# Kernel tuning notes

Measured on AMD Instinct MI355X. Metric: run time of the kernel, lower is better.

The kernel has to match this reference:

```python
import jax, jax.numpy as jnp
import numpy as np

N = 50000          # nodes
E = 800000         # edges (avg degree 16)
DIN, DH, DOUT = 128, 256, 40


def setup_inputs() -> dict:
    key = jax.random.key(0)
    ks = jax.random.split(key, 6)
    x = jax.random.normal(ks[0], (N, DIN), dtype=jnp.float32)
    edge_index = jax.random.randint(ks[1], (2, E), 0, N, dtype=jnp.int32)
    W1 = jax.random.normal(ks[2], (DIN, DH), dtype=jnp.float32) * (1.0 / np.sqrt(DIN))
    b1 = jnp.zeros((DH,), dtype=jnp.float32)
    W2 = jax.random.normal(ks[3], (DH, DOUT), dtype=jnp.float32) * (1.0 / np.sqrt(DH))
    b2 = jnp.zeros((DOUT,), dtype=jnp.float32)
    return {"x": x, "edge_index": edge_index, "W1": W1, "b1": b1, "W2": W2, "b2": b2}


def gcn_conv(x, src, dst, W, b, n):
    # PyG GCNConv: add self-loops, symmetric normalization D^-1/2 A D^-1/2,
    # dense projection, scatter-sum aggregation, then bias.
    deg = jax.ops.segment_sum(jnp.ones_like(dst, dtype=x.dtype), dst, num_segments=n)
    dinv = jnp.where(deg > 0, jax.lax.rsqrt(deg), 0.0)
    norm = dinv[src] * dinv[dst]          # [E+N]
    h = x @ W                              # [N, dout] dense GEMM
    msg = h[src] * norm[:, None]          # gather + scale, [E+N, dout]
    out = jax.ops.segment_sum(msg, dst, num_segments=n)  # scatter-add
    return out + b


def reference(x, edge_index, W1, b1, W2, b2):
    n = x.shape[0]
    loops = jnp.arange(n, dtype=edge_index.dtype)
    src = jnp.concatenate([edge_index[0], loops])
    dst = jnp.concatenate([edge_index[1], loops])
    h = jax.nn.relu(gcn_conv(x, src, dst, W1, b1, n))
    h = gcn_conv(h, src, dst, W2, b2, n)
    return jax.nn.log_softmax(h, axis=1)
```

## Files before the change

kernel.cpp:

```cpp
#include <hip/hip_runtime.h>
#include <math.h>

#define DIN 128
#define DH 256
#define DOUT 40
#define MLP_ROWS 64

#define BSH 7
#define BNODES 128
#define NBUK 391
#define CAP 4096
#define PART_T 512
#define PART_EPB 8
#define PART_CHUNK (PART_T * PART_EPB)

typedef short short8 __attribute__((ext_vector_type(8)));
typedef float f32x4 __attribute__((ext_vector_type(4)));

__device__ inline unsigned f2bf(float f) {
    unsigned u = __float_as_uint(f);
    return (u + 0x7fffu + ((u >> 16) & 1u)) >> 16;
}
__device__ inline float bflo(unsigned u) { return __uint_as_float(u << 16); }
__device__ inline float bfhi(unsigned u) { return __uint_as_float(u & 0xffff0000u); }


__global__ __launch_bounds__(PART_T) void k_partition(
    const int* __restrict__ src, const int* __restrict__ dst,
    int* __restrict__ gcur, unsigned* __restrict__ raw, int E) {
    __shared__ int hist[NBUK];
    __shared__ int lbase[NBUK];
    int tid = threadIdx.x;
    int base_e = blockIdx.x * PART_CHUNK;

    for (int i = tid; i < NBUK; i += PART_T) hist[i] = 0;
    __syncthreads();

    int s[PART_EPB], d[PART_EPB];
#pragma unroll
    for (int k = 0; k < PART_EPB; ++k) {
        int e = base_e + k * PART_T + tid;
        if (e < E) { s[k] = src[e]; d[k] = dst[e]; }
        else d[k] = -1;
    }
#pragma unroll
    for (int k = 0; k < PART_EPB; ++k)
        if (d[k] >= 0) atomicAdd(&hist[d[k] >> BSH], 1);
    __syncthreads();

    for (int b = tid; b < NBUK; b += PART_T) {
        int c = hist[b];
        lbase[b] = c ? atomicAdd(&gcur[b], c) : 0;
    }
    __syncthreads();
    for (int i = tid; i < NBUK; i += PART_T) hist[i] = 0;
    __syncthreads();

#pragma unroll
    for (int k = 0; k < PART_EPB; ++k) {
        if (d[k] >= 0) {
            int b = d[k] >> BSH;
            int pos = lbase[b] + atomicAdd(&hist[b], 1);
            if (pos < (b + 1) * CAP)
                raw[pos] = ((unsigned)(d[k] & (BNODES - 1)) << 16) | (unsigned)s[k];
        }
    }
}

__global__ __launch_bounds__(256) void k_bucket_csr(
    const unsigned* __restrict__ raw, const int* __restrict__ gcur,
    int* __restrict__ row_ptr, int* __restrict__ row_end,
    float* __restrict__ dinv, unsigned short* __restrict__ esrc, int n) {
    __shared__ int cnt[BNODES];
    __shared__ int scn[BNODES];
    __shared__ int lcur[BNODES];
    int b = blockIdx.x;
    int tid = threadIdx.x;
    int base = b * CAP;
    int size = gcur[b] - base;
    if (size > CAP) size = CAP;

    if (tid < BNODES) cnt[tid] = 0;
    __syncthreads();
    for (int i = tid; i < size; i += 256)
        atomicAdd(&cnt[raw[base + i] >> 16], 1);
    __syncthreads();

    if (tid < BNODES) scn[tid] = cnt[tid];
    __syncthreads();
    for (int off = 1; off < BNODES; off <<= 1) {
        int v = 0;
        if (tid < BNODES && tid >= off) v = scn[tid - off];
        __syncthreads();
        if (tid < BNODES) scn[tid] += v;
        __syncthreads();
    }
    if (tid < BNODES) {
        int excl = scn[tid] - cnt[tid];
        lcur[tid] = excl;
        int g = b * BNODES + tid;
        if (g < n) {
            row_ptr[g] = base + excl;
            row_end[g] = base + excl + cnt[tid];
            dinv[g]    = rsqrtf((float)cnt[tid] + 1.0f);
        }
    }
    __syncthreads();
    for (int i = tid; i < size; i += 256) {
        unsigned rec = raw[base + i];
        int pos = atomicAdd(&lcur[rec >> 16], 1);
        esrc[base + pos] = (unsigned short)(rec & 0xffffu);
    }
}

__global__ void k_prep(const float* __restrict__ x, const float* __restrict__ W1,
                       const float* __restrict__ W2, unsigned* __restrict__ xb,
                       unsigned* __restrict__ w1t, unsigned* __restrict__ w2t,
                       int* __restrict__ gcur, int n64) {
    int i = blockIdx.x * blockDim.x + threadIdx.x;
    if (i < n64) {
        float2 v = ((const float2*)x)[i];
        xb[i] = f2bf(v.x) | (f2bf(v.y) << 16);
        return;
    }
    i -= n64;
    if (i < 256 * 64) {
        int c = i >> 6;
        int kk = (i & 63) * 2;
        w1t[i] = f2bf(W1[kk * DH + c]) | (f2bf(W1[(kk + 1) * DH + c]) << 16);
        return;
    }
    i -= 256 * 64;
    if (i < 48 * 128) {
        int col = i >> 7;
        int kk = (i & 127) * 2;
        float a = (col < DOUT) ? W2[kk * DOUT + col] : 0.f;
        float bb = (col < DOUT) ? W2[(kk + 1) * DOUT + col] : 0.f;
        w2t[i] = f2bf(a) | (f2bf(bb) << 16);
        return;
    }
    i -= 48 * 128;
    if (i < NBUK) gcur[i] = i * CAP;
}

__global__ void k_gather_agg1(const uint2* __restrict__ xb2,
                              const unsigned short* __restrict__ esrc,
                              const int* __restrict__ row_ptr, const int* __restrict__ row_end,
                              const float* __restrict__ dinv, uint2* __restrict__ axb2, int n) {
    int wid = (blockIdx.x * blockDim.x + threadIdx.x) >> 6;
    int lane = threadIdx.x & 63;
    int node = wid * 2 + (lane >> 5);
    int hl = lane & 31;
    if (node >= n) return;
    int beg = row_ptr[node], end = row_end[node];
    float dn = dinv[node];
    uint2 sv = xb2[(size_t)node * 32 + hl];
    float ax = dn * bflo(sv.x), ay = dn * bfhi(sv.x);
    float az = dn * bflo(sv.y), aw = dn * bfhi(sv.y);
    int t = beg;
    for (; t + 8 <= end; t += 8) {
        int s0 = esrc[t],     s1 = esrc[t + 1], s2 = esrc[t + 2], s3 = esrc[t + 3];
        int s4 = esrc[t + 4], s5 = esrc[t + 5], s6 = esrc[t + 6], s7 = esrc[t + 7];
        float w0 = dinv[s0], w1 = dinv[s1], w2 = dinv[s2], w3 = dinv[s3];
        float w4 = dinv[s4], w5 = dinv[s5], w6 = dinv[s6], w7 = dinv[s7];
        uint2 v0 = xb2[(size_t)s0 * 32 + hl];
        uint2 v1 = xb2[(size_t)s1 * 32 + hl];
        uint2 v2 = xb2[(size_t)s2 * 32 + hl];
        uint2 v3 = xb2[(size_t)s3 * 32 + hl];
        uint2 v4 = xb2[(size_t)s4 * 32 + hl];
        uint2 v5 = xb2[(size_t)s5 * 32 + hl];
        uint2 v6 = xb2[(size_t)s6 * 32 + hl];
        uint2 v7 = xb2[(size_t)s7 * 32 + hl];
        ax += w0 * bflo(v0.x) + w1 * bflo(v1.x) + w2 * bflo(v2.x) + w3 * bflo(v3.x)
            + w4 * bflo(v4.x) + w5 * bflo(v5.x) + w6 * bflo(v6.x) + w7 * bflo(v7.x);
        ay += w0 * bfhi(v0.x) + w1 * bfhi(v1.x) + w2 * bfhi(v2.x) + w3 * bfhi(v3.x)
            + w4 * bfhi(v4.x) + w5 * bfhi(v5.x) + w6 * bfhi(v6.x) + w7 * bfhi(v7.x);
        az += w0 * bflo(v0.y) + w1 * bflo(v1.y) + w2 * bflo(v2.y) + w3 * bflo(v3.y)
            + w4 * bflo(v4.y) + w5 * bflo(v5.y) + w6 * bflo(v6.y) + w7 * bflo(v7.y);
        aw += w0 * bfhi(v0.y) + w1 * bfhi(v1.y) + w2 * bfhi(v2.y) + w3 * bfhi(v3.y)
            + w4 * bfhi(v4.y) + w5 * bfhi(v5.y) + w6 * bfhi(v6.y) + w7 * bfhi(v7.y);
    }
    for (; t + 4 <= end; t += 4) {
        int s0 = esrc[t], s1 = esrc[t + 1], s2 = esrc[t + 2], s3 = esrc[t + 3];
        float w0 = dinv[s0], w1 = dinv[s1], w2 = dinv[s2], w3 = dinv[s3];
        uint2 v0 = xb2[(size_t)s0 * 32 + hl];
        uint2 v1 = xb2[(size_t)s1 * 32 + hl];
        uint2 v2 = xb2[(size_t)s2 * 32 + hl];
        uint2 v3 = xb2[(size_t)s3 * 32 + hl];
        ax += w0 * bflo(v0.x) + w1 * bflo(v1.x) + w2 * bflo(v2.x) + w3 * bflo(v3.x);
        ay += w0 * bfhi(v0.x) + w1 * bfhi(v1.x) + w2 * bfhi(v2.x) + w3 * bfhi(v3.x);
        az += w0 * bflo(v0.y) + w1 * bflo(v1.y) + w2 * bflo(v2.y) + w3 * bflo(v3.y);
        aw += w0 * bfhi(v0.y) + w1 * bfhi(v1.y) + w2 * bfhi(v2.y) + w3 * bfhi(v3.y);
    }
    for (; t < end; ++t) {
        int s = esrc[t];
        float w = dinv[s];
        uint2 v = xb2[(size_t)s * 32 + hl];
        ax += w * bflo(v.x); ay += w * bfhi(v.x);
        az += w * bflo(v.y); aw += w * bfhi(v.y);
    }
    ax *= dn; ay *= dn; az *= dn; aw *= dn;
    axb2[(size_t)node * 32 + hl] =
        make_uint2(f2bf(ax) | (f2bf(ay) << 16), f2bf(az) | (f2bf(aw) << 16));
}

__global__ __launch_bounds__(256) void k_mlp_mfma(
    const unsigned short* __restrict__ axb, const unsigned short* __restrict__ w1t,
    const float* __restrict__ b1, const unsigned short* __restrict__ w2t,
    unsigned short* __restrict__ pb, int n) {
    __shared__ __align__(16) char smem[65536];
    const int tid = threadIdx.x;
    const int lane = tid & 63;
    const int wv = tid >> 6;
    const int l15 = lane & 15;
    const int lg = lane >> 4;
    const int blockRow = blockIdx.x * MLP_ROWS;

    for (int i = tid; i < 256 * 16; i += 256) {
        int j = i >> 4, seg = i & 15;
        short8 v = *(const short8*)(w1t + j * 128 + seg * 8);
        *(short8*)(smem + j * 256 + ((seg * 16) ^ ((j & 7) << 4))) = v;
    }

    int arow = blockRow + wv * 16 + l15;
    if (arow >= n) arow = n - 1;
    const unsigned short* axp = axb + (size_t)arow * DIN + lg * 8;
    short8 aF[4];
#pragma unroll
    for (int ks = 0; ks < 4; ++ks) aF[ks] = *(const short8*)(axp + ks * 32);

    __syncthreads();

    f32x4 acc[16];
#pragma unroll
    for (int nt = 0; nt < 16; ++nt) acc[nt] = (f32x4){0.f, 0.f, 0.f, 0.f};
#pragma unroll
    for (int ks = 0; ks < 4; ++ks) {
        int kb = (ks * 32 + lg * 8) * 2;
#pragma unroll
        for (int nt = 0; nt < 16; ++nt) {
            int j = nt * 16 + l15;
            short8 bF = *(const short8*)(smem + j * 256 + (kb ^ ((j & 7) << 4)));
            acc[nt] = __builtin_amdgcn_mfma_f32_16x16x32_bf16(aF[ks], bF, acc[nt], 0, 0, 0);
        }
    }
    __syncthreads();

    unsigned short* s_h = (unsigned short*)smem;
    unsigned short* s_w2 = (unsigned short*)(smem + 33792);

#pragma unroll
    for (int nt = 0; nt < 16; ++nt) {
        int col = nt * 16 + l15;
        float bias = b1[col];
#pragma unroll
        for (int r = 0; r < 4; ++r) {
            int row = wv * 16 + lg * 4 + r;
            float v = fmaxf(acc[nt][r] + bias, 0.f);
            s_h[row * 264 + col] = (unsigned short)f2bf(v);
        }
    }
    for (int i = tid; i < 48 * 32; i += 256) {
        int j = i >> 5, seg = i & 31;
        short8 v = *(const short8*)(w2t + j * 256 + seg * 8);
        *(short8*)(s_w2 + j * 264 + seg * 8) = v;
    }
    __syncthreads();

    f32x4 acc2[3];
#pragma unroll
    for (int t = 0; t < 3; ++t) acc2[t] = (f32x4){0.f, 0.f, 0.f, 0.f};
#pragma unroll
    for (int ks = 0; ks < 8; ++ks) {
        int k = ks * 32 + lg * 8;
        short8 aH = *(const short8*)(s_h + (wv * 16 + l15) * 264 + k);
#pragma unroll
        for (int t = 0; t < 3; ++t) {
            short8 bF = *(const short8*)(s_w2 + (t * 16 + l15) * 264 + k);
            acc2[t] = __builtin_amdgcn_mfma_f32_16x16x32_bf16(aH, bF, acc2[t], 0, 0, 0);
        }
    }
#pragma unroll
    for (int t = 0; t < 3; ++t) {
        int col = t * 16 + l15;
        if (col < DOUT) {
#pragma unroll
            for (int r = 0; r < 4; ++r) {
                int row = blockRow + wv * 16 + lg * 4 + r;
                if (row < n) pb[(size_t)row * DOUT + col] = (unsigned short)f2bf(acc2[t][r]);
            }
        }
    }
}

__global__ void k_gather2_lsm(const unsigned* __restrict__ pbu,
                              const unsigned short* __restrict__ esrc,
                              const int* __restrict__ row_ptr, const int* __restrict__ row_end,
                              const float* __restrict__ dinv, const float* __restrict__ b2,
                              float* __restrict__ out, int n) {
    int wid = (blockIdx.x * blockDim.x + threadIdx.x) >> 6;
    int lane = threadIdx.x & 63;
    int node = wid * 2 + (lane >> 5);
    int hl = lane & 31;
    if (node >= n) return;
    int beg = row_ptr[node], end = row_end[node];
    float dn = dinv[node];
    int cl = (hl < 20) ? hl : 0;
    unsigned pv = pbu[(size_t)node * 20 + cl];
    float accx = dn * bflo(pv);
    float accy = dn * bfhi(pv);
    int t = beg;
    for (; t + 8 <= end; t += 8) {
        int s0 = esrc[t],     s1 = esrc[t + 1], s2 = esrc[t + 2], s3 = esrc[t + 3];
        int s4 = esrc[t + 4], s5 = esrc[t + 5], s6 = esrc[t + 6], s7 = esrc[t + 7];
        float w0 = dinv[s0], w1 = dinv[s1], w2 = dinv[s2], w3 = dinv[s3];
        float w4 = dinv[s4], w5 = dinv[s5], w6 = dinv[s6], w7 = dinv[s7];
        unsigned p0 = pbu[(size_t)s0 * 20 + cl];
        unsigned p1 = pbu[(size_t)s1 * 20 + cl];
        unsigned p2 = pbu[(size_t)s2 * 20 + cl];
        unsigned p3 = pbu[(size_t)s3 * 20 + cl];
        unsigned p4 = pbu[(size_t)s4 * 20 + cl];
        unsigned p5 = pbu[(size_t)s5 * 20 + cl];
        unsigned p6 = pbu[(size_t)s6 * 20 + cl];
        unsigned p7 = pbu[(size_t)s7 * 20 + cl];
        accx += w0 * bflo(p0) + w1 * bflo(p1) + w2 * bflo(p2) + w3 * bflo(p3)
              + w4 * bflo(p4) + w5 * bflo(p5) + w6 * bflo(p6) + w7 * bflo(p7);
        accy += w0 * bfhi(p0) + w1 * bfhi(p1) + w2 * bfhi(p2) + w3 * bfhi(p3)
              + w4 * bfhi(p4) + w5 * bfhi(p5) + w6 * bfhi(p6) + w7 * bfhi(p7);
    }
    for (; t + 4 <= end; t += 4) {
        int s0 = esrc[t], s1 = esrc[t + 1], s2 = esrc[t + 2], s3 = esrc[t + 3];
        float w0 = dinv[s0], w1 = dinv[s1], w2 = dinv[s2], w3 = dinv[s3];
        unsigned p0 = pbu[(size_t)s0 * 20 + cl];
        unsigned p1 = pbu[(size_t)s1 * 20 + cl];
        unsigned p2 = pbu[(size_t)s2 * 20 + cl];
        unsigned p3 = pbu[(size_t)s3 * 20 + cl];
        accx += w0 * bflo(p0) + w1 * bflo(p1) + w2 * bflo(p2) + w3 * bflo(p3);
        accy += w0 * bfhi(p0) + w1 * bfhi(p1) + w2 * bfhi(p2) + w3 * bfhi(p3);
    }
    for (; t < end; ++t) {
        int s = esrc[t];
        float w = dinv[s];
        unsigned p = pbu[(size_t)s * 20 + cl];
        accx += w * bflo(p);
        accy += w * bfhi(p);
    }
    float vx = -INFINITY, vy = -INFINITY;
    if (hl < 20) {
        float2 bv = ((const float2*)b2)[hl];
        vx = dn * accx + bv.x;
        vy = dn * accy + bv.y;
    }
    float m = fmaxf(vx, vy);
#pragma unroll
    for (int off = 16; off; off >>= 1) m = fmaxf(m, __shfl_xor(m, off, 32));
    float ex = (hl < 20) ? (expf(vx - m) + expf(vy - m)) : 0.f;
    float ssum = ex;
#pragma unroll
    for (int off = 16; off; off >>= 1) ssum += __shfl_xor(ssum, off, 32);
    float ls = logf(ssum);
    if (hl < 20)
        ((float2*)(out + (size_t)node * DOUT))[hl] = make_float2(vx - m - ls, vy - m - ls);
}

extern "C" void kernel_launch(void* const* d_in, const int* in_sizes, int n_in,
                              void* d_out, int out_size, void* d_ws, size_t ws_size,
                              hipStream_t stream) {
    const float* x  = (const float*)d_in[0];
    const int*   ei = (const int*)d_in[1];
    const float* W1 = (const float*)d_in[2];
    const float* b1 = (const float*)d_in[3];
    const float* W2 = (const float*)d_in[4];
    const float* b2 = (const float*)d_in[5];
    float* out = (float*)d_out;

    int n = in_sizes[0] / DIN;
    int E = in_sizes[1] / 2;
    const int* src = ei;
    const int* dst = ei + E;

    int*            gcur    = (int*)d_ws;
    int*            row_ptr = gcur + 512;
    int*            row_end = row_ptr + n;
    float*          dinv    = (float*)(row_end + n);
    unsigned*       w1t     = (unsigned*)(dinv + n);
    unsigned*       w2t     = w1t + 16384;
    unsigned*       raw     = w2t + 6144;
    unsigned short* esrc    = (unsigned short*)(raw + (size_t)NBUK * CAP);
    unsigned*       xb      = (unsigned*)(esrc + (size_t)NBUK * CAP);
    unsigned*       axb     = xb + (size_t)n * 64;
    unsigned short* pb      = (unsigned short*)xb;

    const int B = 256;
    int part_blocks = (E + PART_CHUNK - 1) / PART_CHUNK;
    int prep_items = n * 64 + 256 * 64 + 48 * 128 + NBUK;
    int npairs = (n + 1) / 2;
    int gath_blocks = (int)(((size_t)npairs * 64 + B - 1) / B);

    k_prep<<<(prep_items + B - 1) / B, B, 0, stream>>>(x, W1, W2, xb, w1t, w2t, gcur, n * 64);
    k_partition<<<part_blocks, PART_T, 0, stream>>>(src, dst, gcur, raw, E);
    k_bucket_csr<<<NBUK, B, 0, stream>>>(raw, gcur, row_ptr, row_end, dinv, esrc, n);
    k_gather_agg1<<<gath_blocks, B, 0, stream>>>(
        (const uint2*)xb, esrc, row_ptr, row_end, dinv, (uint2*)axb, n);
    k_mlp_mfma<<<(n + MLP_ROWS - 1) / MLP_ROWS, B, 0, stream>>>(
        (const unsigned short*)axb, (const unsigned short*)w1t, b1,
        (const unsigned short*)w2t, pb, n);
    k_gather2_lsm<<<gath_blocks, B, 0, stream>>>(
        (const unsigned*)pb, esrc, row_ptr, row_end, dinv, b2, out, n);
}
```

Before: 114.5 us.

## Fuse prep into partition kernel, pad CSR rows to 8, vectorize edge-index loads

Merges the bf16 conversion/weight-transpose prep kernel into the edge partition kernel via a grid-stride loop, and replaces the gcur initialisation with a memset (gcur now holds per-bucket offsets rather than absolute positions). Pads each CSR row start to a multiple of 8 so the gather kernels can load 8 or 16 uint16 source indices with one or two uint4 loads, and unrolls the gathers to 16 edges. Halves edges per partition block to get more blocks. Padding can overflow the bucket CAP for dense buckets, which is clamped and could drop edges; it also adds a memset launch.

```diff
diff --git a/kernel.cpp b/kernel.cpp
--- a/kernel.cpp
+++ b/kernel.cpp
@@ -11,7 +11,7 @@
 #define NBUK 391
 #define CAP 4096
 #define PART_T 512
-#define PART_EPB 8
+#define PART_EPB 4
 #define PART_CHUNK (PART_T * PART_EPB)
 
 typedef short short8 __attribute__((ext_vector_type(8)));
@@ -24,15 +24,38 @@
 __device__ inline float bflo(unsigned u) { return __uint_as_float(u << 16); }
 __device__ inline float bfhi(unsigned u) { return __uint_as_float(u & 0xffff0000u); }
 
-
-__global__ __launch_bounds__(PART_T) void k_partition(
-    const int* __restrict__ src, const int* __restrict__ dst,
-    int* __restrict__ gcur, unsigned* __restrict__ raw, int E) {
+__global__ __launch_bounds__(PART_T) void k_prep_part(
+    const float* __restrict__ x, const float* __restrict__ W1,
+    const float* __restrict__ W2, const int* __restrict__ src,
+    const int* __restrict__ dst, unsigned* __restrict__ xb,
+    unsigned* __restrict__ w1t, unsigned* __restrict__ w2t,
+    int* __restrict__ gcur, unsigned* __restrict__ raw, int E, int n64) {
     __shared__ int hist[NBUK];
     __shared__ int lbase[NBUK];
     int tid = threadIdx.x;
+
+    int prep_items = n64 + 256 * 64 + 48 * 128;
+    int gsize = gridDim.x * PART_T;
+    for (int i = blockIdx.x * PART_T + tid; i < prep_items; i += gsize) {
+        if (i < n64) {
+            float2 v = ((const float2*)x)[i];
+            xb[i] = f2bf(v.x) | (f2bf(v.y) << 16);
+        } else if (i < n64 + 256 * 64) {
+            int j = i - n64;
+            int c = j >> 6;
+            int kk = (j & 63) * 2;
+            w1t[j] = f2bf(W1[kk * DH + c]) | (f2bf(W1[(kk + 1) * DH + c]) << 16);
+        } else {
+            int j = i - n64 - 256 * 64;
+            int col = j >> 7;
+            int kk = (j & 127) * 2;
+            float a = (col < DOUT) ? W2[kk * DOUT + col] : 0.f;
+            float bb = (col < DOUT) ? W2[(kk + 1) * DOUT + col] : 0.f;
+            w2t[j] = f2bf(a) | (f2bf(bb) << 16);
+        }
+    }
+
     int base_e = blockIdx.x * PART_CHUNK;
-
     for (int i = tid; i < NBUK; i += PART_T) hist[i] = 0;
     __syncthreads();
 
@@ -50,7 +73,7 @@
 
     for (int b = tid; b < NBUK; b += PART_T) {
         int c = hist[b];
-        lbase[b] = c ? atomicAdd(&gcur[b], c) : 0;
+        lbase[b] = b * CAP + (c ? atomicAdd(&gcur[b], c) : 0);
     }
     __syncthreads();
     for (int i = tid; i < NBUK; i += PART_T) hist[i] = 0;
@@ -77,7 +100,7 @@
     int b = blockIdx.x;
     int tid = threadIdx.x;
     int base = b * CAP;
-    int size = gcur[b] - base;
+    int size = gcur[b];
     if (size > CAP) size = CAP;
 
     if (tid < BNODES) cnt[tid] = 0;
@@ -86,7 +109,7 @@
         atomicAdd(&cnt[raw[base + i] >> 16], 1);
     __syncthreads();
 
-    if (tid < BNODES) scn[tid] = cnt[tid];
+    if (tid < BNODES) scn[tid] = (cnt[tid] + 7) & ~7;
     __syncthreads();
     for (int off = 1; off < BNODES; off <<= 1) {
         int v = 0;
@@ -96,12 +119,16 @@
         __syncthreads();
     }
     if (tid < BNODES) {
-        int excl = scn[tid] - cnt[tid];
+        int c8 = (cnt[tid] + 7) & ~7;
+        int excl = scn[tid] - c8;
+        if (excl > CAP) excl = CAP;
+        int re = excl + cnt[tid];
+        if (re > CAP) re = CAP;
         lcur[tid] = excl;
         int g = b * BNODES + tid;
         if (g < n) {
             row_ptr[g] = base + excl;
-            row_end[g] = base + excl + cnt[tid];
+            row_end[g] = base + re;
             dinv[g]    = rsqrtf((float)cnt[tid] + 1.0f);
         }
     }
@@ -109,38 +136,8 @@
     for (int i = tid; i < size; i += 256) {
         unsigned rec = raw[base + i];
         int pos = atomicAdd(&lcur[rec >> 16], 1);
-        esrc[base + pos] = (unsigned short)(rec & 0xffffu);
-    }
-}
-
-__global__ void k_prep(const float* __restrict__ x, const float* __restrict__ W1,
-                       const float* __restrict__ W2, unsigned* __restrict__ xb,
-                       unsigned* __restrict__ w1t, unsigned* __restrict__ w2t,
-                       int* __restrict__ gcur, int n64) {
-    int i = blockIdx.x * blockDim.x + threadIdx.x;
-    if (i < n64) {
-        float2 v = ((const float2*)x)[i];
-        xb[i] = f2bf(v.x) | (f2bf(v.y) << 16);
-        return;
-    }
-    i -= n64;
-    if (i < 256 * 64) {
-        int c = i >> 6;
-        int kk = (i & 63) * 2;
-        w1t[i] = f2bf(W1[kk * DH + c]) | (f2bf(W1[(kk + 1) * DH + c]) << 16);
-        return;
-    }
-    i -= 256 * 64;
-    if (i < 48 * 128) {
-        int col = i >> 7;
-        int kk = (i & 127) * 2;
-        float a = (col < DOUT) ? W2[kk * DOUT + col] : 0.f;
-        float bb = (col < DOUT) ? W2[(kk + 1) * DOUT + col] : 0.f;
-        w2t[i] = f2bf(a) | (f2bf(bb) << 16);
-        return;
-    }
-    i -= 48 * 128;
-    if (i < NBUK) gcur[i] = i * CAP;
+        if (pos < CAP) esrc[base + pos] = (unsigned short)(rec & 0xffffu);
+    }
 }
 
 __global__ void k_gather_agg1(const uint2* __restrict__ xb2,
@@ -158,19 +155,52 @@
     float ax = dn * bflo(sv.x), ay = dn * bfhi(sv.x);
     float az = dn * bflo(sv.y), aw = dn * bfhi(sv.y);
     int t = beg;
-    for (; t + 8 <= end; t += 8) {
-        int s0 = esrc[t],     s1 = esrc[t + 1], s2 = esrc[t + 2], s3 = esrc[t + 3];
-        int s4 = esrc[t + 4], s5 = esrc[t + 5], s6 = esrc[t + 6], s7 = esrc[t + 7];
+    for (; t + 16 <= end; t += 16) {
+        uint4 q0 = *(const uint4*)(esrc + t);
+        uint4 q1 = *(const uint4*)(esrc + t + 8);
+        int s0 = q0.x & 0xffff, s1 = q0.x >> 16, s2 = q0.y & 0xffff, s3 = q0.y >> 16;
+        int s4 = q0.z & 0xffff, s5 = q0.z >> 16, s6 = q0.w & 0xffff, s7 = q0.w >> 16;
+        int s8 = q1.x & 0xffff, s9 = q1.x >> 16, sa = q1.y & 0xffff, sb = q1.y >> 16;
+        int sc = q1.z & 0xffff, sd = q1.z >> 16, se = q1.w & 0xffff, sf = q1.w >> 16;
         float w0 = dinv[s0], w1 = dinv[s1], w2 = dinv[s2], w3 = dinv[s3];
         float w4 = dinv[s4], w5 = dinv[s5], w6 = dinv[s6], w7 = dinv[s7];
-        uint2 v0 = xb2[(size_t)s0 * 32 + hl];
-        uint2 v1 = xb2[(size_t)s1 * 32 + hl];
-        uint2 v2 = xb2[(size_t)s2 * 32 + hl];
-        uint2 v3 = xb2[(size_t)s3 * 32 + hl];
-        uint2 v4 = xb2[(size_t)s4 * 32 + hl];
-        uint2 v5 = xb2[(size_t)s5 * 32 + hl];
-        uint2 v6 = xb2[(size_t)s6 * 32 + hl];
-        uint2 v7 = xb2[(size_t)s7 * 32 + hl];
+        float w8 = dinv[s8], w9 = dinv[s9], wa = dinv[sa], wb = dinv[sb];
+        float wc = dinv[sc], wd = dinv[sd], we = dinv[se], wf = dinv[sf];
+        uint2 v0 = xb2[(size_t)s0 * 32 + hl], v1 = xb2[(size_t)s1 * 32 + hl];
+        uint2 v2 = xb2[(size_t)s2 * 32 + hl], v3 = xb2[(size_t)s3 * 32 + hl];
+        uint2 v4 = xb2[(size_t)s4 * 32 + hl], v5 = xb2[(size_t)s5 * 32 + hl];
+        uint2 v6 = xb2[(size_t)s6 * 32 + hl], v7 = xb2[(size_t)s7 * 32 + hl];
+        uint2 v8 = xb2[(size_t)s8 * 32 + hl], v9 = xb2[(size_t)s9 * 32 + hl];
+        uint2 va = xb2[(size_t)sa * 32 + hl], vb = xb2[(size_t)sb * 32 + hl];
+        uint2 vc = xb2[(size_t)sc * 32 + hl], vd = xb2[(size_t)sd * 32 + hl];
+        uint2 ve = xb2[(size_t)se * 32 + hl], vf = xb2[(size_t)sf * 32 + hl];
+        ax += w0 * bflo(v0.x) + w1 * bflo(v1.x) + w2 * bflo(v2.x) + w3 * bflo(v3.x)
+            + w4 * bflo(v4.x) + w5 * bflo(v5.x) + w6 * bflo(v6.x) + w7 * bflo(v7.x)
+            + w8 * bflo(v8.x) + w9 * bflo(v9.x) + wa * bflo(va.x) + wb * bflo(vb.x)
+            + wc * bflo(vc.x) + wd * bflo(vd.x) + we * bflo(ve.x) + wf * bflo(vf.x);
+        ay += w0 * bfhi(v0.x) + w1 * bfhi(v1.x) + w2 * bfhi(v2.x) + w3 * bfhi(v3.x)
+            + w4 * bfhi(v4.x) + w5 * bfhi(v5.x) + w6 * bfhi(v6.x) + w7 * bfhi(v7.x)
+            + w8 * bfhi(v8.x) + w9 * bfhi(v9.x) + wa * bfhi(va.x) + wb * bfhi(vb.x)
+            + wc * bfhi(vc.x) + wd * bfhi(vd.x) + we * bfhi(ve.x) + wf * bfhi(vf.x);
+        az += w0 * bflo(v0.y) + w1 * bflo(v1.y) + w2 * bflo(v2.y) + w3 * bflo(v3.y)
+            + w4 * bflo(v4.y) + w5 * bflo(v5.y) + w6 * bflo(v6.y) + w7 * bflo(v7.y)
+            + w8 * bflo(v8.y) + w9 * bflo(v9.y) + wa * bflo(va.y) + wb * bflo(vb.y)
+            + wc * bflo(vc.y) + wd * bflo(vd.y) + we * bflo(ve.y) + wf * bflo(vf.y);
+        aw += w0 * bfhi(v0.y) + w1 * bfhi(v1.y) + w2 * bfhi(v2.y) + w3 * bfhi(v3.y)
+            + w4 * bfhi(v4.y) + w5 * bfhi(v5.y) + w6 * bfhi(v6.y) + w7 * bfhi(v7.y)
+            + w8 * bfhi(v8.y) + w9 * bfhi(v9.y) + wa * bfhi(va.y) + wb * bfhi(vb.y)
+            + wc * bfhi(vc.y) + wd * bfhi(vd.y) + we * bfhi(ve.y) + wf * bfhi(vf.y);
+    }
+    for (; t + 8 <= end; t += 8) {
+        uint4 q0 = *(const uint4*)(esrc + t);
+        int s0 = q0.x & 0xffff, s1 = q0.x >> 16, s2 = q0.y & 0xffff, s3 = q0.y >> 16;
+        int s4 = q0.z & 0xffff, s5 = q0.z >> 16, s6 = q0.w & 0xffff, s7 = q0.w >> 16;
+        float w0 = dinv[s0], w1 = dinv[s1], w2 = dinv[s2], w3 = dinv[s3];
+        float w4 = dinv[s4], w5 = dinv[s5], w6 = dinv[s6], w7 = dinv[s7];
+        uint2 v0 = xb2[(size_t)s0 * 32 + hl], v1 = xb2[(size_t)s1 * 32 + hl];
+        uint2 v2 = xb2[(size_t)s2 * 32 + hl], v3 = xb2[(size_t)s3 * 32 + hl];
+        uint2 v4 = xb2[(size_t)s4 * 32 + hl], v5 = xb2[(size_t)s5 * 32 + hl];
+        uint2 v6 = xb2[(size_t)s6 * 32 + hl], v7 = xb2[(size_t)s7 * 32 + hl];
         ax += w0 * bflo(v0.x) + w1 * bflo(v1.x) + w2 * bflo(v2.x) + w3 * bflo(v3.x)
             + w4 * bflo(v4.x) + w5 * bflo(v5.x) + w6 * bflo(v6.x) + w7 * bflo(v7.x);
         ay += w0 * bfhi(v0.x) + w1 * bfhi(v1.x) + w2 * bfhi(v2.x) + w3 * bfhi(v3.x)
@@ -179,18 +209,6 @@
             + w4 * bflo(v4.y) + w5 * bflo(v5.y) + w6 * bflo(v6.y) + w7 * bflo(v7.y);
         aw += w0 * bfhi(v0.y) + w1 * bfhi(v1.y) + w2 * bfhi(v2.y) + w3 * bfhi(v3.y)
             + w4 * bfhi(v4.y) + w5 * bfhi(v5.y) + w6 * bfhi(v6.y) + w7 * bfhi(v7.y);
-    }
-    for (; t + 4 <= end; t += 4) {
-        int s0 = esrc[t], s1 = esrc[t + 1], s2 = esrc[t + 2], s3 = esrc[t + 3];
-        float w0 = dinv[s0], w1 = dinv[s1], w2 = dinv[s2], w3 = dinv[s3];
-        uint2 v0 = xb2[(size_t)s0 * 32 + hl];
-        uint2 v1 = xb2[(size_t)s1 * 32 + hl];
-        uint2 v2 = xb2[(size_t)s2 * 32 + hl];
-        uint2 v3 = xb2[(size_t)s3 * 32 + hl];
-        ax += w0 * bflo(v0.x) + w1 * bflo(v1.x) + w2 * bflo(v2.x) + w3 * bflo(v3.x);
-        ay += w0 * bfhi(v0.x) + w1 * bfhi(v1.x) + w2 * bfhi(v2.x) + w3 * bfhi(v3.x);
-        az += w0 * bflo(v0.y) + w1 * bflo(v1.y) + w2 * bflo(v2.y) + w3 * bflo(v3.y);
-        aw += w0 * bfhi(v0.y) + w1 * bfhi(v1.y) + w2 * bfhi(v2.y) + w3 * bfhi(v3.y);
     }
     for (; t < end; ++t) {
         int s = esrc[t];
@@ -310,33 +328,48 @@
     float accx = dn * bflo(pv);
     float accy = dn * bfhi(pv);
     int t = beg;
-    for (; t + 8 <= end; t += 8) {
-        int s0 = esrc[t],     s1 = esrc[t + 1], s2 = esrc[t + 2], s3 = esrc[t + 3];
-        int s4 = esrc[t + 4], s5 = esrc[t + 5], s6 = esrc[t + 6], s7 = esrc[t + 7];
+    for (; t + 16 <= end; t += 16) {
+        uint4 q0 = *(const uint4*)(esrc + t);
+        uint4 q1 = *(const uint4*)(esrc + t + 8);
+        int s0 = q0.x & 0xffff, s1 = q0.x >> 16, s2 = q0.y & 0xffff, s3 = q0.y >> 16;
+        int s4 = q0.z & 0xffff, s5 = q0.z >> 16, s6 = q0.w & 0xffff, s7 = q0.w >> 16;
+        int s8 = q1.x & 0xffff, s9 = q1.x >> 16, sa = q1.y & 0xffff, sb = q1.y >> 16;
+        int sc = q1.z & 0xffff, sd = q1.z >> 16, se = q1.w & 0xffff, sf = q1.w >> 16;
         float w0 = dinv[s0], w1 = dinv[s1], w2 = dinv[s2], w3 = dinv[s3];
         float w4 = dinv[s4], w5 = dinv[s5], w6 = dinv[s6], w7 = dinv[s7];
-        unsigned p0 = pbu[(size_t)s0 * 20 + cl];
-        unsigned p1 = pbu[(size_t)s1 * 20 + cl];
-        unsigned p2 = pbu[(size_t)s2 * 20 + cl];
-        unsigned p3 = pbu[(size_t)s3 * 20 + cl];
-        unsigned p4 = pbu[(size_t)s4 * 20 + cl];
-        unsigned p5 = pbu[(size_t)s5 * 20 + cl];
-        unsigned p6 = pbu[(size_t)s6 * 20 + cl];
-        unsigned p7 = pbu[(size_t)s7 * 20 + cl];
+        float w8 = dinv[s8], w9 = dinv[s9], wa = dinv[sa], wb = dinv[sb];
+        float wc = dinv[sc], wd = dinv[sd], we = dinv[se], wf = dinv[sf];
+        unsigned p0 = pbu[(size_t)s0 * 20 + cl], p1 = pbu[(size_t)s1 * 20 + cl];
+        unsigned p2 = pbu[(size_t)s2 * 20 + cl], p3 = pbu[(size_t)s3 * 20 + cl];
+        unsigned p4 = pbu[(size_t)s4 * 20 + cl], p5 = pbu[(size_t)s5 * 20 + cl];
+        unsigned p6 = pbu[(size_t)s6 * 20 + cl], p7 = pbu[(size_t)s7 * 20 + cl];
+        unsigned p8 = pbu[(size_t)s8 * 20 + cl], p9 = pbu[(size_t)s9 * 20 + cl];
+        unsigned pa = pbu[(size_t)sa * 20 + cl], pb_ = pbu[(size_t)sb * 20 + cl];
+        unsigned pc = pbu[(size_t)sc * 20 + cl], pd = pbu[(size_t)sd * 20 + cl];
+        unsigned pe = pbu[(size_t)se * 20 + cl], pf = pbu[(size_t)sf * 20 + cl];
+        accx += w0 * bflo(p0) + w1 * bflo(p1) + w2 * bflo(p2) + w3 * bflo(p3)
+              + w4 * bflo(p4) + w5 * bflo(p5) + w6 * bflo(p6) + w7 * bflo(p7)
+              + w8 * bflo(p8) + w9 * bflo(p9) + wa * bflo(pa) + wb * bflo(pb_)
+              + wc * bflo(pc) + wd * bflo(pd) + we * bflo(pe) + wf * bflo(pf);
+        accy += w0 * bfhi(p0) + w1 * bfhi(p1) + w2 * bfhi(p2) + w3 * bfhi(p3)
+              + w4 * bfhi(p4) + w5 * bfhi(p5) + w6 * bfhi(p6) + w7 * bfhi(p7)
+              + w8 * bfhi(p8) + w9 * bfhi(p9) + wa * bfhi(pa) + wb * bfhi(pb_)
+              + wc * bfhi(pc) + wd * bfhi(pd) + we * bfhi(pe) + wf * bfhi(pf);
+    }
+    for (; t + 8 <= end; t += 8) {
+        uint4 q0 = *(const uint4*)(esrc + t);
+        int s0 = q0.x & 0xffff, s1 = q0.x >> 16, s2 = q0.y & 0xffff, s3 = q0.y >> 16;
+        int s4 = q0.z & 0xffff, s5 = q0.z >> 16, s6 = q0.w & 0xffff, s7 = q0.w >> 16;
+        float w0 = dinv[s0], w1 = dinv[s1], w2 = dinv[s2], w3 = dinv[s3];
+        float w4 = dinv[s4], w5 = dinv[s5], w6 = dinv[s6], w7 = dinv[s7];
+        unsigned p0 = pbu[(size_t)s0 * 20 + cl], p1 = pbu[(size_t)s1 * 20 + cl];
+        unsigned p2 = pbu[(size_t)s2 * 20 + cl], p3 = pbu[(size_t)s3 * 20 + cl];
+        unsigned p4 = pbu[(size_t)s4 * 20 + cl], p5 = pbu[(size_t)s5 * 20 + cl];
+        unsigned p6 = pbu[(size_t)s6 * 20 + cl], p7 = pbu[(size_t)s7 * 20 + cl];
         accx += w0 * bflo(p0) + w1 * bflo(p1) + w2 * bflo(p2) + w3 * bflo(p3)
               + w4 * bflo(p4) + w5 * bflo(p5) + w6 * bflo(p6) + w7 * bflo(p7);
         accy += w0 * bfhi(p0) + w1 * bfhi(p1) + w2 * bfhi(p2) + w3 * bfhi(p3)
               + w4 * bfhi(p4) + w5 * bfhi(p5) + w6 * bfhi(p6) + w7 * bfhi(p7);
-    }
-    for (; t + 4 <= end; t += 4) {
-        int s0 = esrc[t], s1 = esrc[t + 1], s2 = esrc[t + 2], s3 = esrc[t + 3];
-        float w0 = dinv[s0], w1 = dinv[s1], w2 = dinv[s2], w3 = dinv[s3];
-        unsigned p0 = pbu[(size_t)s0 * 20 + cl];
-        unsigned p1 = pbu[(size_t)s1 * 20 + cl];
-        unsigned p2 = pbu[(size_t)s2 * 20 + cl];
-        unsigned p3 = pbu[(size_t)s3 * 20 + cl];
-        accx += w0 * bflo(p0) + w1 * bflo(p1) + w2 * bflo(p2) + w3 * bflo(p3);
-        accy += w0 * bfhi(p0) + w1 * bfhi(p1) + w2 * bfhi(p2) + w3 * bfhi(p3);
     }
     for (; t < end; ++t) {
         int s = esrc[t];
@@ -393,12 +426,12 @@
 
     const int B = 256;
     int part_blocks = (E + PART_CHUNK - 1) / PART_CHUNK;
-    int prep_items = n * 64 + 256 * 64 + 48 * 128 + NBUK;
     int npairs = (n + 1) / 2;
     int gath_blocks = (int)(((size_t)npairs * 64 + B - 1) / B);
 
-    k_prep<<<(prep_items + B - 1) / B, B, 0, stream>>>(x, W1, W2, xb, w1t, w2t, gcur, n * 64);
-    k_partition<<<part_blocks, PART_T, 0, stream>>>(src, dst, gcur, raw, E);
+    hipMemsetAsync(gcur, 0, NBUK * sizeof(int), stream);
+    k_prep_part<<<part_blocks, PART_T, 0, stream>>>(
+        x, W1, W2, src, dst, xb, w1t, w2t, gcur, raw, E, n * 64);
     k_bucket_csr<<<NBUK, B, 0, stream>>>(raw, gcur, row_ptr, row_end, dinv, esrc, n);
     k_gather_agg1<<<gath_blocks, B, 0, stream>>>(
         (const uint2*)xb, esrc, row_ptr, row_end, dinv, (uint2*)axb, n);
```

Result: slower. 127.9 us (+11.7%).
